# Kernel optimization log

Hardware: AMD Instinct MI355X
Metric: run time of the kernel (lower is better)

Reference implementation:

```python
import jax, jax.numpy as jnp
import numpy as np

HEADS, DIM_HEAD, K_NN, EMB = 4, 64, 16, 256
INNER = HEADS * DIM_HEAD  # 256
POS_HID = 64
ATTN_HID = 4 * DIM_HEAD  # per-head hidden of grouped 1x1 conv MLP


def setup_inputs() -> dict:
    key = jax.random.key(0)
    ks = jax.random.split(key, 16)
    b, n = 2, 4096
    s = 0.05
    inp = {
        "x": jax.random.normal(ks[0], (b, n, EMB), jnp.float32),
        "mask": jnp.ones((b, n), dtype=bool),
        "pos": jax.random.normal(ks[1], (b, n, 3), jnp.float32),
        # to_qkv (no bias)
        "Wqkv": jax.random.normal(ks[2], (EMB, 3 * INNER), jnp.float32) * s,
        # pos_mlp: Linear(3,64) -> ReLU -> Linear(64, inner)
        "Wp1": jax.random.normal(ks[3], (3, POS_HID), jnp.float32) * s,
        "bp1": jax.random.normal(ks[4], (POS_HID,), jnp.float32) * s,
        "Wp2": jax.random.normal(ks[5], (POS_HID, INNER), jnp.float32) * s,
        "bp2": jax.random.normal(ks[6], (INNER,), jnp.float32) * s,
        # attn_mlp: grouped 1x1 convs == per-head linears [h, d_in, d_out]
        "Wa1": jax.random.normal(ks[7], (HEADS, DIM_HEAD, ATTN_HID), jnp.float32) * s,
        "ba1": jax.random.normal(ks[8], (HEADS, ATTN_HID), jnp.float32) * s,
        "Wa2": jax.random.normal(ks[9], (HEADS, ATTN_HID, DIM_HEAD), jnp.float32) * s,
        "ba2": jax.random.normal(ks[10], (HEADS, DIM_HEAD), jnp.float32) * s,
        # to_out
        "Wo": jax.random.normal(ks[11], (INNER, EMB), jnp.float32) * s,
        "bo": jax.random.normal(ks[12], (EMB,), jnp.float32) * s,
    }
    return inp


def reference(x, mask, pos, Wqkv, Wp1, bp1, Wp2, bp2, Wa1, ba1, Wa2, ba2, Wo, bo):
    b, n, _ = x.shape
    h, dh = HEADS, DIM_HEAD

    qkv = x @ Wqkv                              # [b, n, 3*inner]
    q, k, v = jnp.split(qkv, 3, axis=-1)
    to_heads = lambda t: t.reshape(b, n, h, dh).transpose(0, 2, 1, 3)  # [b,h,n,d]
    q, k, v = to_heads(q), to_heads(k), to_heads(v)

    # kNN on pos (per batch, squared euclidean, includes self)
    sq = jnp.sum(pos * pos, axis=-1)
    d2 = sq[:, :, None] + sq[:, None, :] - 2.0 * jnp.einsum('bid,bjd->bij', pos, pos)
    idx = jax.lax.top_k(-d2, K_NN)[1]            # [b, n, K]

    gat_h = jax.vmap(lambda t, i: t[:, i])       # [h,n,d],[n,K] -> [h,n,K,d]
    gat = jax.vmap(lambda t, i: t[i])            # [n,c],[n,K]  -> [n,K,c]

    qg = gat_h(q, idx)                           # [b,h,n,K,d]
    kg = gat_h(k, idx)
    vg = gat_h(v, idx)

    rel = gat(pos, idx) - pos[:, :, None, :]     # [b,n,K,3]
    rpe = jax.nn.relu(rel @ Wp1 + bp1) @ Wp2 + bp2               # [b,n,K,inner]
    rpe = rpe.reshape(b, n, K_NN, h, dh).transpose(0, 3, 1, 2, 4)  # [b,h,n,K,d]

    attn_in = qg - kg + rpe                      # [b,h,n,K,d]
    hid = jax.nn.relu(jnp.einsum('bhnkd,hde->bhnke', attn_in, Wa1)
                      + ba1[None, :, None, None, :])
    sim = (jnp.einsum('bhnke,hed->bhnkd', hid, Wa2)
           + ba2[None, :, None, None, :])        # [b,h,n,K,d]

    mg = jax.vmap(lambda m, i: m[i])(mask, idx)  # [b,n,K]
    pair = (mask[:, :, None] & mg)[:, None, :, :, None]
    sim = jnp.where(pair, sim, -jnp.finfo(sim.dtype).max)

    attn = jax.nn.softmax(sim, axis=3)           # over neighbors j
    # F.normalize over dim=-2 of [b,(h d),i,j] == over the point axis i
    attn = attn / jnp.maximum(jnp.linalg.norm(attn, axis=2, keepdims=True), 1e-12)

    agg = jnp.sum(attn * (vg + rpe), axis=3)     # [b,h,n,d]
    agg = agg.transpose(0, 2, 1, 3).reshape(b, n, h * dh)
    return agg @ Wo + bo
```

## Files before the change

kernel.cpp:

```cpp
#include <hip/hip_runtime.h>
#include <float.h>

typedef unsigned int uint;
typedef unsigned short ushort;

typedef _Float16 f16x8 __attribute__((ext_vector_type(8)));
typedef float f32x4 __attribute__((ext_vector_type(4)));
#define MFMA_F16(A, B, C) __builtin_amdgcn_mfma_f32_16x16x32_f16(A, B, C, 0, 0, 0)

__device__ __forceinline__ ushort f2h(float f) {
    _Float16 h = (_Float16)f;
    return __builtin_bit_cast(ushort, h);
}
__device__ __forceinline__ float h2f(ushort u) {
    _Float16 h = __builtin_bit_cast(_Float16, u);
    return (float)h;
}
__device__ __forceinline__ uint pack2(float a, float b) {
    return (uint)f2h(a) | ((uint)f2h(b) << 16);
}
__device__ __forceinline__ f16x8 cast8(uint4 u) {
    return __builtin_bit_cast(f16x8, u);
}

template <int CTRL>
__device__ __forceinline__ void dpp_min(float& v, int& j) {
    int vp = __builtin_amdgcn_update_dpp(__float_as_int(v), __float_as_int(v),
                                         CTRL, 0xF, 0xF, false);
    int jp = __builtin_amdgcn_update_dpp(j, j, CTRL, 0xF, 0xF, false);
    float vf = __int_as_float(vp);
    bool better = (vf < v) || (vf == v && jp < j);
    v = better ? vf : v;
    j = better ? jp : j;
}
__device__ __forceinline__ void wave_min(float& v, int& j) {
    dpp_min<0x121>(v, j);
    dpp_min<0x122>(v, j);
    dpp_min<0x124>(v, j);
    dpp_min<0x128>(v, j);
    float ov = __shfl_xor(v, 16);
    int oj = __shfl_xor(j, 16);
    bool better = (ov < v) || (ov == v && oj < j);
    v = better ? ov : v;
    j = better ? oj : j;
    ov = __shfl_xor(v, 32);
    oj = __shfl_xor(j, 32);
    better = (ov < v) || (ov == v && oj < j);
    v = better ? ov : v;
    j = better ? oj : j;
}

__global__ void prep_kernel(const float* __restrict__ Wqkv, const float* __restrict__ Wa1,
                            const float* __restrict__ Wa2, const float* __restrict__ Wo,
                            const float* __restrict__ Wp2, const float* __restrict__ ba1,
                            ushort* __restrict__ WcatT, ushort* __restrict__ Wa1T,
                            ushort* __restrict__ Wa2T, ushort* __restrict__ WoT,
                            ushort* __restrict__ Wp2T, ushort* __restrict__ ba1p) {
    int t = blockIdx.x * 256 + threadIdx.x;
    {
        int cc2 = t >> 8, kk = t & 255;
        float val;
        if (cc2 < 256) val = Wqkv[kk * 768 + cc2] - Wqkv[kk * 768 + 256 + cc2];
        else           val = Wqkv[kk * 768 + 256 + cc2];
        WcatT[t] = f2h(val);
    }
    if (t < 65536) {
        int hh = t >> 14, r = t & 16383;
        int e = r >> 6, kin = r & 63;
        Wa1T[t] = f2h(Wa1[((size_t)(hh * 64 + kin)) * 256 + e]);
        int d = r >> 8, pos = r & 255;
        int ec = pos >> 5, lg = (pos >> 3) & 3, q = pos & 7;
        int e2 = ec * 32 + ((q >> 2) & 1) * 16 + lg * 4 + (q & 3);
        Wa2T[t] = f2h(Wa2[((size_t)(hh * 256 + e2)) * 64 + d]);
        int c3 = t >> 8, k3 = t & 255;
        WoT[t] = f2h(Wo[k3 * 256 + c3]);
    }
    if (t < 16384) {
        int row = t >> 6, p = t & 63;
        int h = row >> 6, s = row & 63;
        int ct = s >> 4, rr = s & 15;
        int d = (ct >> 1) * 32 + ((rr >> 2) & 3) * 8 + (ct & 1) * 4 + (rr & 3);
        Wp2T[t] = f2h(Wp2[p * 256 + h * 64 + d]);
    }
    if (t < 1024) {
        int h = t >> 8, pos = t & 255;
        int ec = pos >> 5, lg = (pos >> 3) & 3, q = pos & 7;
        int e2 = ec * 32 + ((q >> 2) & 1) * 16 + lg * 4 + (q & 3);
        ba1p[t] = f2h(ba1[h * 256 + e2]);
    }
}

__global__ void pos4_kernel(const float* __restrict__ pos, float4* __restrict__ pos4) {
    int t = blockIdx.x * 256 + threadIdx.x;
    float x = pos[t * 3 + 0], y = pos[t * 3 + 1], z = pos[t * 3 + 2];
    float4 o = {x, y, z, x * x + y * y + z * z};
    pos4[t] = o;
}

template <int MODE>
__global__ __launch_bounds__(256)
void hgemm(const void* __restrict__ Av, const ushort* __restrict__ Bt,
           const float* __restrict__ bias, void* __restrict__ C0v, ushort* __restrict__ C1h) {
    __shared__ ushort Af[64 * 40];
    __shared__ ushort Bf[128 * 40];
    const int tid = threadIdx.x;
    const int l = tid & 63, wv = tid >> 6;
    const int lg = l >> 4, lr = l & 15;
    const int row0 = blockIdx.x * 64, col0 = blockIdx.y * 128;
    const int mrow = (wv >> 1) * 32, ncol = (wv & 1) * 64;
    f32x4 acc[2][4];
#pragma unroll
    for (int mt = 0; mt < 2; ++mt)
#pragma unroll
        for (int nt = 0; nt < 4; ++nt) acc[mt][nt] = (f32x4){0.f, 0.f, 0.f, 0.f};

    for (int kk = 0; kk < 256; kk += 32) {
        if (MODE == 0) {
            const float* A = (const float*)Av;
            int r = tid >> 2, kq = (tid & 3) * 8;
            float4 a0 = *(const float4*)&A[(size_t)(row0 + r) * 256 + kk + kq];
            float4 a1 = *(const float4*)&A[(size_t)(row0 + r) * 256 + kk + kq + 4];
            uint4 u;
            u.x = pack2(a0.x, a0.y); u.y = pack2(a0.z, a0.w);
            u.z = pack2(a1.x, a1.y); u.w = pack2(a1.z, a1.w);
            *(uint4*)&Af[r * 40 + kq] = u;
        } else {
            const ushort* Ah = (const ushort*)Av;
            int r = tid >> 2, kq = (tid & 3) * 8;
            *(uint4*)&Af[r * 40 + kq] = *(const uint4*)&Ah[(size_t)(row0 + r) * 256 + kk + kq];
        }
        {
            int r = tid >> 1, hh = (tid & 1) * 16;
            const uint4* src = (const uint4*)&Bt[(size_t)(col0 + r) * 256 + kk + hh];
            uint4 b0 = src[0], b1 = src[1];
            *(uint4*)&Bf[r * 40 + hh] = b0;
            *(uint4*)&Bf[r * 40 + hh + 8] = b1;
        }
        __syncthreads();
        f16x8 afr[2], bfr[4];
#pragma unroll
        for (int mt = 0; mt < 2; ++mt)
            afr[mt] = *(const f16x8*)&Af[(mrow + mt * 16 + lr) * 40 + lg * 8];
#pragma unroll
        for (int nt = 0; nt < 4; ++nt)
            bfr[nt] = *(const f16x8*)&Bf[(ncol + nt * 16 + lr) * 40 + lg * 8];
#pragma unroll
        for (int mt = 0; mt < 2; ++mt)
#pragma unroll
            for (int nt = 0; nt < 4; ++nt)
                acc[mt][nt] = MFMA_F16(afr[mt], bfr[nt], acc[mt][nt]);
        __syncthreads();
    }
#pragma unroll
    for (int mt = 0; mt < 2; ++mt)
#pragma unroll
        for (int nt = 0; nt < 4; ++nt)
#pragma unroll
            for (int j = 0; j < 4; ++j) {
                int m = row0 + mrow + mt * 16 + lg * 4 + j;
                int n = col0 + ncol + nt * 16 + lr;
                float v = acc[mt][nt][j];
                if (MODE == 1) {
                    ((float*)C0v)[(size_t)m * 256 + n] = v + bias[n];
                } else {
                    int b = m >> 12, i2 = m & 4095;
                    if (n < 256) {
                        int hh = n >> 6, d = n & 63;
                        ((ushort*)C0v)[((size_t)((b * 4 + hh) << 12) + i2) * 64 + d] = f2h(v);
                    } else {
                        int n2 = n - 256;
                        int hh = n2 >> 6, d = n2 & 63;
                        C1h[((size_t)((b * 4 + hh) << 12) + i2) * 64 + d] = f2h(v);
                    }
                }
            }
}

__global__ __launch_bounds__(256, 6)
void knn_kernel(const float4* __restrict__ pos4, int* __restrict__ idx_out) {
    const int tid = threadIdx.x;
    const int lane = tid & 63, wv = tid >> 6;
    const int pblk = blockIdx.x;
    const int b = pblk >> 10;
    const int i = ((pblk & 1023) << 2) + wv;
    const float4* p4 = pos4 + (size_t)b * 4096;
    float4 pi = p4[i];
    float xi = pi.x, yi = pi.y, zi = pi.z, sqi = pi.w;

    float cm4[4];
    int cj4[4];
#pragma unroll
    for (int g = 0; g < 4; ++g) { cm4[g] = FLT_MAX; cj4[g] = 0x7fffffff; }
#pragma unroll 4
    for (int m = 0; m < 64; ++m) {
        int j = m * 64 + lane;
        float4 pj = p4[j];
        float v = sqi + pj.w - 2.f * (xi * pj.x + yi * pj.y + zi * pj.z);
        int g = m & 3;
        bool better = (v < cm4[g]) || (v == cm4[g] && j < cj4[g]);
        cm4[g] = better ? v : cm4[g];
        cj4[g] = better ? j : cj4[g];
    }
    float cm = cm4[0];
    int cj = cj4[0];
#pragma unroll
    for (int g = 1; g < 4; ++g) {
        bool better = (cm4[g] < cm) || (cm4[g] == cm && cj4[g] < cj);
        cm = better ? cm4[g] : cm;
        cj = better ? cj4[g] : cj;
    }

    unsigned long long extr = 0ull;
    int keep = 0;
#pragma unroll 1
    for (int r = 0; r < 16; ++r) {
        float bv = cm;
        int bj = cj;
        wave_min(bv, bj);
        if (lane == r) keep = bj;
        int c = bj & 63;
        int j = lane * 64 + c;
        float4 pj = p4[j];
        float v = sqi + pj.w - 2.f * (xi * pj.x + yi * pj.y + zi * pj.z);
        bool dead = (((extr >> c) & 1ull) != 0ull) | (j == bj);
        if (j == bj) extr |= (1ull << c);
        v = dead ? FLT_MAX : v;
        int nj = j;
        wave_min(v, nj);
        if (lane == c) { cm = v; cj = nj; }
    }
    if (lane < 16)
        idx_out[((size_t)b * 4096 + i) * 16 + lane] = keep;
}

__global__ __launch_bounds__(256)
void attn_mfma(const ushort* __restrict__ qmkh, const ushort* __restrict__ vbufh,
               const float* __restrict__ pos, const int* __restrict__ idxb,
               const ushort* __restrict__ Wa1Tg, const ushort* __restrict__ Wa2Tg,
               const ushort* __restrict__ Wp2Tg, const ushort* __restrict__ ba1p,
               const float* __restrict__ ba2,
               const float* __restrict__ Wp1, const float* __restrict__ bp1,
               const float* __restrict__ bp2,
               ushort* __restrict__ prodbuf, float* __restrict__ part) {
    __shared__ ushort W1[256 * 72];
    __shared__ ushort W2[64 * 264];
    __shared__ ushort scr[4][16 * 88];
    const int tid = threadIdx.x;
    const int l = tid & 63, wv = tid >> 6;
    const int lg = l >> 4, lr = l & 15;
    const int c = blockIdx.x;
    const int h = c >> 8, rc = c & 255, b = rc >> 7, chunk = rc & 127;
    const int bh = b * 4 + h;

    {
        const uint4* g1 = (const uint4*)(Wa1Tg + (size_t)h * 16384);
        const uint4* g2 = (const uint4*)(Wa2Tg + (size_t)h * 16384);
#pragma unroll
        for (int it = 0; it < 8; ++it) {
            int ci = it * 256 + tid;
            *(uint4*)&W1[(ci >> 3) * 72 + (ci & 7) * 8] = g1[ci];
        }
#pragma unroll
        for (int it = 0; it < 8; ++it) {
            int ci = it * 256 + tid;
            *(uint4*)&W2[(ci >> 5) * 264 + (ci & 31) * 8] = g2[ci];
        }
    }
    __syncthreads();

    float b2v[4];
#pragma unroll
    for (int dt = 0; dt < 4; ++dt) b2v[dt] = ba2[h * 64 + dt * 16 + lr];

    f16x8 wp2f[4][2];
#pragma unroll
    for (int ct = 0; ct < 4; ++ct)
#pragma unroll
        for (int kt = 0; kt < 2; ++kt)
            wp2f[ct][kt] = *(const f16x8*)&Wp2Tg[(size_t)(h * 64 + ct * 16 + lr) * 64 + kt * 32 + lg * 8];
    f16x8 wp1h[3][2], bp1h[2], bp2h[2];
#pragma unroll
    for (int cc = 0; cc < 3; ++cc)
#pragma unroll
        for (int kt = 0; kt < 2; ++kt) {
            float4 w0 = *(const float4*)&Wp1[cc * 64 + kt * 32 + lg * 8];
            float4 w1 = *(const float4*)&Wp1[cc * 64 + kt * 32 + lg * 8 + 4];
            f16x8 wv8;
            wv8[0] = (_Float16)w0.x; wv8[1] = (_Float16)w0.y;
            wv8[2] = (_Float16)w0.z; wv8[3] = (_Float16)w0.w;
            wv8[4] = (_Float16)w1.x; wv8[5] = (_Float16)w1.y;
            wv8[6] = (_Float16)w1.z; wv8[7] = (_Float16)w1.w;
            wp1h[cc][kt] = wv8;
        }
#pragma unroll
    for (int kt = 0; kt < 2; ++kt) {
        float4 b0 = *(const float4*)&bp1[kt * 32 + lg * 8];
        float4 b1 = *(const float4*)&bp1[kt * 32 + lg * 8 + 4];
        f16x8 bv8;
        bv8[0] = (_Float16)b0.x; bv8[1] = (_Float16)b0.y;
        bv8[2] = (_Float16)b0.z; bv8[3] = (_Float16)b0.w;
        bv8[4] = (_Float16)b1.x; bv8[5] = (_Float16)b1.y;
        bv8[6] = (_Float16)b1.z; bv8[7] = (_Float16)b1.w;
        bp1h[kt] = bv8;
        float4 c0 = *(const float4*)&bp2[h * 64 + kt * 32 + lg * 8];
        float4 c1 = *(const float4*)&bp2[h * 64 + kt * 32 + lg * 8 + 4];
        f16x8 cv8;
        cv8[0] = (_Float16)c0.x; cv8[1] = (_Float16)c0.y;
        cv8[2] = (_Float16)c0.z; cv8[3] = (_Float16)c0.w;
        cv8[4] = (_Float16)c1.x; cv8[5] = (_Float16)c1.y;
        cv8[6] = (_Float16)c1.z; cv8[7] = (_Float16)c1.w;
        bp2h[kt] = cv8;
    }
    const float* pb = pos + (size_t)b * 4096 * 3;
    const ushort* qbase = qmkh + (size_t)bh * 4096 * 64;
    const ushort* vbase = vbufh + (size_t)bh * 4096 * 64;
    const ushort* b1base = ba1p + h * 256;
    ushort* sw = &scr[wv][0];

    float asq[4][4];
#pragma unroll
    for (int dt = 0; dt < 4; ++dt)
#pragma unroll
        for (int j2 = 0; j2 < 4; ++j2) asq[dt][j2] = 0.f;

    for (int pg = 0; pg < 2; ++pg) {
        const int i0 = chunk * 32 + pg * 16 + wv * 4;
        int jj[4];
        f16x8 ain[4][2], rpef[4][2];
#pragma unroll
        for (int pp = 0; pp < 4; ++pp) {
            int i = i0 + pp;
            int row = ((b << 12) + i) * 16 + lr;
            int j = idxb[row];
            jj[pp] = j;
            float rx = pb[j * 3 + 0] - pb[i * 3 + 0];
            float ry = pb[j * 3 + 1] - pb[i * 3 + 1];
            float rz = pb[j * 3 + 2] - pb[i * 3 + 2];
            _Float16 rxh = (_Float16)rx, ryh = (_Float16)ry, rzh = (_Float16)rz;
            f16x8 hf[2];
#pragma unroll
            for (int kt = 0; kt < 2; ++kt) {
                f16x8 t = bp1h[kt] + rxh * wp1h[0][kt] + ryh * wp1h[1][kt] + rzh * wp1h[2][kt];
#pragma unroll
                for (int q = 0; q < 8; ++q) t[q] = t[q] > (_Float16)0.f ? t[q] : (_Float16)0.f;
                hf[kt] = t;
            }
            f32x4 z4 = {0.f, 0.f, 0.f, 0.f};
            f32x4 racc[4];
#pragma unroll
            for (int ct = 0; ct < 4; ++ct) {
                racc[ct] = MFMA_F16(wp2f[ct][0], hf[0], z4);
                racc[ct] = MFMA_F16(wp2f[ct][1], hf[1], racc[ct]);
            }
            const ushort* qb = qbase + ((size_t)j) * 64 + lg * 8;
#pragma unroll
            for (int kt = 0; kt < 2; ++kt) {
                uint4 rp;
                rp.x = pack2(racc[2 * kt][0], racc[2 * kt][1]);
                rp.y = pack2(racc[2 * kt][2], racc[2 * kt][3]);
                rp.z = pack2(racc[2 * kt + 1][0], racc[2 * kt + 1][1]);
                rp.w = pack2(racc[2 * kt + 1][2], racc[2 * kt + 1][3]);
                f16x8 rv = cast8(rp) + bp2h[kt];
                rpef[pp][kt] = rv;
                f16x8 qv = *(const f16x8*)(qb + kt * 32);
                ain[pp][kt] = qv + rv;
            }
        }
        f32x4 acc[4][4];
#pragma unroll
        for (int pp = 0; pp < 4; ++pp)
#pragma unroll
            for (int dt = 0; dt < 4; ++dt) acc[pp][dt] = (f32x4){0.f, 0.f, 0.f, 0.f};

        for (int ec = 0; ec < 8; ++ec) {
            f16x8 A1[2][2], B2f[4];
#pragma unroll
            for (int et = 0; et < 2; ++et)
#pragma unroll
                for (int kt = 0; kt < 2; ++kt)
                    A1[et][kt] = *(const f16x8*)&W1[(ec * 32 + et * 16 + lr) * 72 + kt * 32 + lg * 8];
#pragma unroll
            for (int dt = 0; dt < 4; ++dt)
                B2f[dt] = *(const f16x8*)&W2[(dt * 16 + lr) * 264 + ec * 32 + lg * 8];
            f16x8 b1h = *(const f16x8*)&b1base[ec * 32 + lg * 8];
#pragma unroll
            for (int pp = 0; pp < 4; ++pp) {
                f32x4 z = {0.f, 0.f, 0.f, 0.f};
                f32x4 h0 = MFMA_F16(A1[0][0], ain[pp][0], z);
                h0 = MFMA_F16(A1[0][1], ain[pp][1], h0);
                f32x4 h1 = MFMA_F16(A1[1][0], ain[pp][0], z);
                h1 = MFMA_F16(A1[1][1], ain[pp][1], h1);
                uint4 hp;
                hp.x = pack2(h0[0], h0[1]); hp.y = pack2(h0[2], h0[3]);
                hp.z = pack2(h1[0], h1[1]); hp.w = pack2(h1[2], h1[3]);
                f16x8 hv = cast8(hp) + b1h;
#pragma unroll
                for (int q = 0; q < 8; ++q) hv[q] = hv[q] > (_Float16)0.f ? hv[q] : (_Float16)0.f;
#pragma unroll
                for (int dt = 0; dt < 4; ++dt)
                    acc[pp][dt] = MFMA_F16(hv, B2f[dt], acc[pp][dt]);
            }
        }
#pragma unroll
        for (int pp = 0; pp < 4; ++pp) {
            int i = i0 + pp;
            float at[4][4];
#pragma unroll
            for (int dt = 0; dt < 4; ++dt) {
                float v0 = acc[pp][dt][0] + b2v[dt];
                float v1 = acc[pp][dt][1] + b2v[dt];
                float v2 = acc[pp][dt][2] + b2v[dt];
                float v3 = acc[pp][dt][3] + b2v[dt];
                float m = fmaxf(fmaxf(v0, v1), fmaxf(v2, v3));
                m = fmaxf(m, __shfl_xor(m, 16));
                m = fmaxf(m, __shfl_xor(m, 32));
                float e0 = __expf(v0 - m), e1 = __expf(v1 - m);
                float e2 = __expf(v2 - m), e3 = __expf(v3 - m);
                float s = e0 + e1 + e2 + e3;
                s += __shfl_xor(s, 16);
                s += __shfl_xor(s, 32);
                float is = 1.f / s;
                at[dt][0] = e0 * is; at[dt][1] = e1 * is;
                at[dt][2] = e2 * is; at[dt][3] = e3 * is;
                asq[dt][0] += at[dt][0] * at[dt][0];
                asq[dt][1] += at[dt][1] * at[dt][1];
                asq[dt][2] += at[dt][2] * at[dt][2];
                asq[dt][3] += at[dt][3] * at[dt][3];
            }
#pragma unroll
            for (int dt = 0; dt < 4; ++dt) {
                sw[(lg * 4 + 0) * 88 + dt * 16 + lr] = f2h(at[dt][0]);
                sw[(lg * 4 + 1) * 88 + dt * 16 + lr] = f2h(at[dt][1]);
                sw[(lg * 4 + 2) * 88 + dt * 16 + lr] = f2h(at[dt][2]);
                sw[(lg * 4 + 3) * 88 + dt * 16 + lr] = f2h(at[dt][3]);
            }
            const ushort* vb = vbase + (size_t)jj[pp] * 64 + lg * 8;
            ushort* pr = prodbuf + ((size_t)(bh * 4096 + i) * 16 + lr) * 64 + lg * 8;
#pragma unroll
            for (int kt = 0; kt < 2; ++kt) {
                f16x8 atB = *(const f16x8*)&sw[lr * 88 + kt * 32 + lg * 8];
                f16x8 vv = *(const f16x8*)(vb + kt * 32);
                f16x8 p = (vv + rpef[pp][kt]) * atB;
                *(f16x8*)(pr + kt * 32) = p;
            }
        }
    }
    float* scrF = (float*)&scr[0][0];
#pragma unroll
    for (int dt = 0; dt < 4; ++dt) {
        __syncthreads();
#pragma unroll
        for (int j2 = 0; j2 < 4; ++j2)
            scrF[wv * 288 + lr * 18 + lg * 4 + j2] = asq[dt][j2];
        __syncthreads();
        int fr = tid >> 4, fk = tid & 15;
        float s = scrF[fr * 18 + fk] + scrF[288 + fr * 18 + fk] +
                  scrF[576 + fr * 18 + fk] + scrF[864 + fr * 18 + fk];
        part[((size_t)c * 4 + dt) * 256 + tid] = s;
    }
}

__global__ void inv_kernel(const float* __restrict__ part, float* __restrict__ invn) {
    int t = blockIdx.x * 256 + threadIdx.x;
    int bh = t >> 10, f = t & 1023;
    int d = f >> 4, k = f & 15;
    int dt = d >> 4, lr = d & 15;
    int cbase = (bh & 3) * 256 + (bh >> 2) * 128;
    float s = 0.f;
    for (int cc = 0; cc < 128; ++cc)
        s += part[((size_t)(cbase + cc) * 4 + dt) * 256 + lr * 16 + k];
    invn[t] = 1.f / fmaxf(sqrtf(s), 1e-12f);
}

__global__ void finalize_kernel(const ushort* __restrict__ prodbuf, const float* __restrict__ invn,
                                ushort* __restrict__ aggh) {
    int t = blockIdx.x * 256 + threadIdx.x;
    int d = t & 63;
    int i = (t >> 6) & 4095;
    int bh = t >> 18;
    const ushort* pr = prodbuf + ((size_t)(bh * 4096 + i)) * 1024 + d;
    const float* iv = invn + bh * 1024 + d * 16;
    float accv = 0.f;
#pragma unroll
    for (int k = 0; k < 16; ++k)
        accv += h2f(pr[(size_t)k * 64]) * iv[k];
    int hh = bh & 3, bb = bh >> 2;
    aggh[((size_t)(bb * 4096 + i)) * 256 + hh * 64 + d] = f2h(accv);
}

extern "C" void kernel_launch(void* const* d_in, const int* in_sizes, int n_in,
                              void* d_out, int out_size, void* d_ws, size_t ws_size,
                              hipStream_t stream) {
    const float* x    = (const float*)d_in[0];
    const float* pos  = (const float*)d_in[2];
    const float* Wqkv = (const float*)d_in[3];
    const float* Wp1  = (const float*)d_in[4];
    const float* bp1  = (const float*)d_in[5];
    const float* Wp2  = (const float*)d_in[6];
    const float* bp2  = (const float*)d_in[7];
    const float* Wa1  = (const float*)d_in[8];
    const float* ba1  = (const float*)d_in[9];
    const float* Wa2  = (const float*)d_in[10];
    const float* ba2  = (const float*)d_in[11];
    const float* Wo   = (const float*)d_in[12];
    const float* bo   = (const float*)d_in[13];

    char* base = (char*)d_ws;
    size_t off = 0;
    auto carve = [&](size_t bytes) -> char* {
        char* r = base + off;
        off = (off + bytes + 255) & ~(size_t)255;
        return r;
    };
    ushort* qmkh   = (ushort*)carve(4194304);
    ushort* vbufh  = (ushort*)carve(4194304);
    ushort* WcatT  = (ushort*)carve(262144);
    ushort* Wa1Tg  = (ushort*)carve(131072);
    ushort* Wa2Tg  = (ushort*)carve(131072);
    ushort* WoT    = (ushort*)carve(131072);
    ushort* Wp2Tg  = (ushort*)carve(32768);
    ushort* ba1pg  = (ushort*)carve(2048);
    float4* pos4   = (float4*)carve(131072);
    int*    idx    = (int*)carve(524288);
    ushort* prodbuf= (ushort*)carve(67108864);
    float*  part   = (float*)carve(4194304);
    float*  invn   = (float*)carve(32768);
    ushort* aggh   = (ushort*)carve(4194304);

    prep_kernel<<<512, 256, 0, stream>>>(Wqkv, Wa1, Wa2, Wo, Wp2, ba1,
                                         WcatT, Wa1Tg, Wa2Tg, WoT, Wp2Tg, ba1pg);
    pos4_kernel<<<32, 256, 0, stream>>>(pos, pos4);
    hgemm<0><<<dim3(128, 4), 256, 0, stream>>>(x, WcatT, nullptr, qmkh, vbufh);
    knn_kernel<<<2048, 256, 0, stream>>>(pos4, idx);
    attn_mfma<<<1024, 256, 0, stream>>>(qmkh, vbufh, pos, idx, Wa1Tg, Wa2Tg, Wp2Tg, ba1pg,
                                        ba2, Wp1, bp1, bp2, prodbuf, part);
    inv_kernel<<<32, 256, 0, stream>>>(part, invn);
    finalize_kernel<<<8192, 256, 0, stream>>>(prodbuf, invn, aggh);
    hgemm<1><<<dim3(128, 2), 256, 0, stream>>>(aggh, WoT, bo, d_out, nullptr);
}
```

Baseline: 190.2 us.

## Read attention MLP weights from global memory instead of LDS staging

Drops the per-block LDS staging of the per-head Wa1/Wa2 weights and its barrier, loading MFMA operand fragments straight from global memory (L1/L2-cached) inside the ec loop. It also switches fp32-to-fp16 packing to the hardware cvt_pkrtz instruction and reads positions as float4 from the precomputed pos4 buffer. This removes LDS footprint and startup latency, which may raise occupancy. The cost is repeated global/cache loads in the inner loop and round-toward-zero instead of round-to-nearest conversion.

```diff
diff --git a/kernel.cpp b/kernel.cpp
--- a/kernel.cpp
+++ b/kernel.cpp
@@ -18,6 +18,9 @@
 }
 __device__ __forceinline__ uint pack2(float a, float b) {
     return (uint)f2h(a) | ((uint)f2h(b) << 16);
+}
+__device__ __forceinline__ uint pkrtz(float a, float b) {
+    return __builtin_bit_cast(uint, __builtin_amdgcn_cvt_pkrtz(a, b));
 }
 __device__ __forceinline__ f16x8 cast8(uint4 u) {
     return __builtin_bit_cast(f16x8, u);
@@ -235,15 +238,13 @@
 
 __global__ __launch_bounds__(256)
 void attn_mfma(const ushort* __restrict__ qmkh, const ushort* __restrict__ vbufh,
-               const float* __restrict__ pos, const int* __restrict__ idxb,
+               const float4* __restrict__ pos4, const int* __restrict__ idxb,
                const ushort* __restrict__ Wa1Tg, const ushort* __restrict__ Wa2Tg,
                const ushort* __restrict__ Wp2Tg, const ushort* __restrict__ ba1p,
                const float* __restrict__ ba2,
                const float* __restrict__ Wp1, const float* __restrict__ bp1,
                const float* __restrict__ bp2,
                ushort* __restrict__ prodbuf, float* __restrict__ part) {
-    __shared__ ushort W1[256 * 72];
-    __shared__ ushort W2[64 * 264];
     __shared__ ushort scr[4][16 * 88];
     const int tid = threadIdx.x;
     const int l = tid & 63, wv = tid >> 6;
@@ -252,21 +253,8 @@
     const int h = c >> 8, rc = c & 255, b = rc >> 7, chunk = rc & 127;
     const int bh = b * 4 + h;
 
-    {
-        const uint4* g1 = (const uint4*)(Wa1Tg + (size_t)h * 16384);
-        const uint4* g2 = (const uint4*)(Wa2Tg + (size_t)h * 16384);
-#pragma unroll
-        for (int it = 0; it < 8; ++it) {
-            int ci = it * 256 + tid;
-            *(uint4*)&W1[(ci >> 3) * 72 + (ci & 7) * 8] = g1[ci];
-        }
-#pragma unroll
-        for (int it = 0; it < 8; ++it) {
-            int ci = it * 256 + tid;
-            *(uint4*)&W2[(ci >> 5) * 264 + (ci & 31) * 8] = g2[ci];
-        }
-    }
-    __syncthreads();
+    const ushort* w1g = Wa1Tg + (size_t)h * 16384;
+    const ushort* w2g = Wa2Tg + (size_t)h * 16384;
 
     float b2v[4];
 #pragma unroll
@@ -311,7 +299,7 @@
         cv8[6] = (_Float16)c1.z; cv8[7] = (_Float16)c1.w;
         bp2h[kt] = cv8;
     }
-    const float* pb = pos + (size_t)b * 4096 * 3;
+    const float4* pb4 = pos4 + (size_t)b * 4096;
     const ushort* qbase = qmkh + (size_t)bh * 4096 * 64;
     const ushort* vbase = vbufh + (size_t)bh * 4096 * 64;
     const ushort* b1base = ba1p + h * 256;
@@ -333,10 +321,11 @@
             int row = ((b << 12) + i) * 16 + lr;
             int j = idxb[row];
             jj[pp] = j;
-            float rx = pb[j * 3 + 0] - pb[i * 3 + 0];
-            float ry = pb[j * 3 + 1] - pb[i * 3 + 1];
-            float rz = pb[j * 3 + 2] - pb[i * 3 + 2];
-            _Float16 rxh = (_Float16)rx, ryh = (_Float16)ry, rzh = (_Float16)rz;
+            float4 pj = pb4[j];
+            float4 pi = pb4[i];
+            _Float16 rxh = (_Float16)(pj.x - pi.x);
+            _Float16 ryh = (_Float16)(pj.y - pi.y);
+            _Float16 rzh = (_Float16)(pj.z - pi.z);
             f16x8 hf[2];
 #pragma unroll
             for (int kt = 0; kt < 2; ++kt) {
@@ -356,10 +345,10 @@
 #pragma unroll
             for (int kt = 0; kt < 2; ++kt) {
                 uint4 rp;
-                rp.x = pack2(racc[2 * kt][0], racc[2 * kt][1]);
-                rp.y = pack2(racc[2 * kt][2], racc[2 * kt][3]);
-                rp.z = pack2(racc[2 * kt + 1][0], racc[2 * kt + 1][1]);
-                rp.w = pack2(racc[2 * kt + 1][2], racc[2 * kt + 1][3]);
+                rp.x = pkrtz(racc[2 * kt][0], racc[2 * kt][1]);
+                rp.y = pkrtz(racc[2 * kt][2], racc[2 * kt][3]);
+                rp.z = pkrtz(racc[2 * kt + 1][0], racc[2 * kt + 1][1]);
+                rp.w = pkrtz(racc[2 * kt + 1][2], racc[2 * kt + 1][3]);
                 f16x8 rv = cast8(rp) + bp2h[kt];
                 rpef[pp][kt] = rv;
                 f16x8 qv = *(const f16x8*)(qb + kt * 32);
@@ -378,10 +367,10 @@
             for (int et = 0; et < 2; ++et)
 #pragma unroll
                 for (int kt = 0; kt < 2; ++kt)
-                    A1[et][kt] = *(const f16x8*)&W1[(ec * 32 + et * 16 + lr) * 72 + kt * 32 + lg * 8];
+                    A1[et][kt] = *(const f16x8*)&w1g[(size_t)(ec * 32 + et * 16 + lr) * 64 + kt * 32 + lg * 8];
 #pragma unroll
             for (int dt = 0; dt < 4; ++dt)
-                B2f[dt] = *(const f16x8*)&W2[(dt * 16 + lr) * 264 + ec * 32 + lg * 8];
+                B2f[dt] = *(const f16x8*)&w2g[(size_t)(dt * 16 + lr) * 256 + ec * 32 + lg * 8];
             f16x8 b1h = *(const f16x8*)&b1base[ec * 32 + lg * 8];
 #pragma unroll
             for (int pp = 0; pp < 4; ++pp) {
@@ -391,8 +380,8 @@
                 f32x4 h1 = MFMA_F16(A1[1][0], ain[pp][0], z);
                 h1 = MFMA_F16(A1[1][1], ain[pp][1], h1);
                 uint4 hp;
-                hp.x = pack2(h0[0], h0[1]); hp.y = pack2(h0[2], h0[3]);
-                hp.z = pack2(h1[0], h1[1]); hp.w = pack2(h1[2], h1[3]);
+                hp.x = pkrtz(h0[0], h0[1]); hp.y = pkrtz(h0[2], h0[3]);
+                hp.z = pkrtz(h1[0], h1[1]); hp.w = pkrtz(h1[2], h1[3]);
                 f16x8 hv = cast8(hp) + b1h;
 #pragma unroll
                 for (int q = 0; q < 8; ++q) hv[q] = hv[q] > (_Float16)0.f ? hv[q] : (_Float16)0.f;
@@ -532,7 +521,7 @@
     pos4_kernel<<<32, 256, 0, stream>>>(pos, pos4);
     hgemm<0><<<dim3(128, 4), 256, 0, stream>>>(x, WcatT, nullptr, qmkh, vbufh);
     knn_kernel<<<2048, 256, 0, stream>>>(pos4, idx);
-    attn_mfma<<<1024, 256, 0, stream>>>(qmkh, vbufh, pos, idx, Wa1Tg, Wa2Tg, Wp2Tg, ba1pg,
+    attn_mfma<<<1024, 256, 0, stream>>>(qmkh, vbufh, pos4, idx, Wa1Tg, Wa2Tg, Wp2Tg, ba1pg,
                                         ba2, Wp1, bp1, bp2, prodbuf, part);
     inv_kernel<<<32, 256, 0, stream>>>(part, invn);
     finalize_kernel<<<8192, 256, 0, stream>>>(prodbuf, invn, aggh);
```

Measured after the change: 213.5 us. 1.12x slower.
